# Kernel optimization log

Hardware: AMD Instinct MI355X
Metric: run time of the kernel (lower is better)

## Reference

```python
import jax, jax.numpy as jnp
import numpy as np

NUM_HEADS = 8
EPS = 1e-12  # torch F.normalize default eps


def _l2norm(t):
    # t / max(||t||_2, eps) along last axis (matches F.normalize)
    n = jnp.sqrt(jnp.sum(t * t, axis=-1, keepdims=True))
    return t / jnp.maximum(n, EPS)


def setup_inputs() -> dict:
    key = jax.random.key(0)
    k1, k2, k3 = jax.random.split(key, 3)
    B, N, C = 8, 1024, 768
    x = jax.random.normal(k1, (B, N, C), dtype=jnp.float32)
    w_qkv = jax.random.normal(k2, (C, 3 * C), dtype=jnp.float32) * 0.02
    temperature = jnp.ones((NUM_HEADS, 1, 1), dtype=jnp.float32)
    w_proj = jax.random.normal(k3, (C, C), dtype=jnp.float32) * 0.02
    b_proj = jnp.zeros((C,), dtype=jnp.float32)
    return {"x": x, "w_qkv": w_qkv, "temperature": temperature,
            "w_proj": w_proj, "b_proj": b_proj}


def reference(x, w_qkv, temperature, w_proj, b_proj):
    B, N, C = x.shape
    H = NUM_HEADS
    hd = C // H
    # qkv projection (no bias), split into q,k,v of shape [B,H,N,hd]
    qkv = (x @ w_qkv).reshape(B, N, 3, H, hd)
    qkv = jnp.transpose(qkv, (2, 0, 3, 1, 4))  # [3,B,H,N,hd]
    q, k, v = qkv[0], qkv[1], qkv[2]
    q = _l2norm(q)
    k = _l2norm(k)
    # NOTE: code (unlike canonical XCA) does NOT transpose q/k, so attn is [B,H,N,N]
    attn = jnp.einsum('bhnd,bhmd->bhnm', q, k) * temperature  # temp broadcasts over B
    attn = jax.nn.softmax(attn, axis=-1)
    out = jnp.einsum('bhnm,bhmd->bhnd', attn, v)  # [B,H,N,hd]
    out = jnp.transpose(out, (0, 2, 1, 3)).reshape(B, N, C)
    return out @ w_proj + b_proj
```

## Files before the change

kernel.cpp:

```cpp
#include <hip/hip_runtime.h>
#include <math.h>

typedef __attribute__((ext_vector_type(8))) short bf16x8;
typedef __attribute__((ext_vector_type(4))) float f32x4;
typedef unsigned short u16;
typedef unsigned int u32;


__device__ __forceinline__ u16 f2b(float f) {
  u32 u = __float_as_uint(f);
  return (u16)((u + 0x7fffu + ((u >> 16) & 1u)) >> 16);
}
__device__ __forceinline__ float b2f(u16 h) {
  return __uint_as_float(((u32)h) << 16);
}
__device__ __forceinline__ int swz(int m) { return (m ^ (m >> 2)) & 3; }

__device__ __forceinline__ void async16(const void* g, void* l) {
  __builtin_amdgcn_global_load_lds((const __attribute__((address_space(1))) u32*)g,
                                   (__attribute__((address_space(3))) u32*)l, 16, 0, 0);
}

__global__ __launch_bounds__(256) void prep_kernel(const float* __restrict__ x,
                                                   const float* __restrict__ w_qkv,
                                                   const float* __restrict__ w_proj,
                                                   u16* __restrict__ xb,
                                                   u16* __restrict__ wqkvT,
                                                   u16* __restrict__ wprojT) {
  __shared__ float t[32][33];
  const int blk = blockIdx.x;
  if (blk < 6144) {
    const int idx = blk * 256 + threadIdx.x;
    const float4 v = ((const float4*)x)[idx];
    uint2 o;
    o.x = (u32)f2b(v.x) | ((u32)f2b(v.y) << 16);
    o.y = (u32)f2b(v.z) | ((u32)f2b(v.w) << 16);
    ((uint2*)xb)[idx] = o;
    return;
  }
  const float* in; u16* out; int R, C, bx, by;
  if (blk < 6144 + 1728) {
    const int rem = blk - 6144;
    in = w_qkv; out = wqkvT; R = 768; C = 2304; bx = rem % 72; by = rem / 72;
  } else {
    const int rem = blk - 6144 - 1728;
    in = w_proj; out = wprojT; R = 768; C = 768; bx = rem % 24; by = rem / 24;
  }
  const int c0 = bx * 32, r0 = by * 32;
  const int tc = threadIdx.x & 31, tr = threadIdx.x >> 5;
#pragma unroll
  for (int j = 0; j < 4; ++j)
    t[tr + j * 8][tc] = in[(size_t)(r0 + tr + j * 8) * C + c0 + tc];
  __syncthreads();
#pragma unroll
  for (int j = 0; j < 4; ++j)
    out[(size_t)(c0 + tr + j * 8) * R + r0 + tc] = f2b(t[tc][tr + j * 8]);
}

template<int NT>
__device__ __forceinline__ void gemm_core(const u16* __restrict__ A,
                                          const u16* __restrict__ Bt,
                                          int m0, int n0, f32x4 acc[4][NT / 32]) {
  constexpr int JT = NT / 32;
  constexpr int NINST = (512 + NT * 4) / 256;
  __shared__ u16 Sm[(512 + NT * 4) * 8];
  const int tid = threadIdx.x;
  const int w = tid >> 6, lane = tid & 63;
  const int i15 = lane & 15, quad = lane >> 4;
  const int wm = (w >> 1) * 64, wn = (w & 1) * (NT / 2);
  const int sw = quad ^ swz(i15);

#pragma unroll
  for (int i = 0; i < 4; ++i)
#pragma unroll
    for (int j = 0; j < JT; ++j) acc[i][j] = (f32x4){0.f, 0.f, 0.f, 0.f};

  for (int k0 = 0; k0 < 768; k0 += 32) {
    __syncthreads();
#pragma unroll
    for (int inst = 0; inst < NINST; ++inst) {
      const int s = inst * 256 + tid;
      const u16* src;
      if (inst < 2) {
        const int m = s >> 2, e = s & 3;
        src = A + ((size_t)(m0 + m) * 768 + k0 + (e ^ swz(m)) * 8);
      } else {
        const int s2 = s - 512;
        const int n = s2 >> 2, e = s2 & 3;
        src = Bt + ((size_t)(n0 + n) * 768 + k0 + (e ^ swz(n)) * 8);
      }
      async16(src, (void*)(Sm + (size_t)(inst * 256 + w * 64) * 8));
    }
    __syncthreads();
    bf16x8 af[4], bf[JT];
#pragma unroll
    for (int i = 0; i < 4; ++i)
      af[i] = *(const bf16x8*)(Sm + ((size_t)(wm + i * 16 + i15) * 4 + sw) * 8);
#pragma unroll
    for (int j = 0; j < JT; ++j)
      bf[j] = *(const bf16x8*)(Sm + ((size_t)512 + (wn + j * 16 + i15) * 4 + sw) * 8);
#pragma unroll
    for (int i = 0; i < 4; ++i)
#pragma unroll
      for (int j = 0; j < JT; ++j)
        acc[i][j] = __builtin_amdgcn_mfma_f32_16x16x32_bf16(af[i], bf[j], acc[i][j], 0, 0, 0);
  }
}

__global__ __launch_bounds__(256, 3) void qkv_gemm_kernel(
    const u16* __restrict__ xb, const u16* __restrict__ wT,
    const float* __restrict__ temp,
    u16* __restrict__ q, u16* __restrict__ k, u16* __restrict__ vT) {
  f32x4 acc[4][6];
  const int bid = blockIdx.x;
  const int xcd = bid & 7, slot = bid >> 3;
  const int mb = xcd * 8 + slot / 12, nb = slot % 12;
  const int m0 = mb * 128, n0 = nb * 192;
  gemm_core<192>(xb, wT, m0, n0, acc);

  const int tid = threadIdx.x, w = tid >> 6, lane = tid & 63;
  const int i15 = lane & 15, quad = lane >> 4;
  const int wm = (w >> 1) * 64;
  const int three = nb >> 2;
  const int h = ((nb & 3) << 1) + (w & 1);

  if (three < 2) {
    u16* dst = three ? k : q;
    const float sc_extra = three ? 1.f : temp[h];
#pragma unroll
    for (int it = 0; it < 4; ++it) {
#pragma unroll
      for (int r = 0; r < 4; ++r) {
        float s = 0.f;
#pragma unroll
        for (int jt = 0; jt < 6; ++jt) s += acc[it][jt][r] * acc[it][jt][r];
        s += __shfl_xor(s, 1); s += __shfl_xor(s, 2);
        s += __shfl_xor(s, 4); s += __shfl_xor(s, 8);
        const float scale = sc_extra / fmaxf(sqrtf(s), 1e-12f);
        const int m = m0 + wm + it * 16 + quad * 4 + r;
        const int b = m >> 10, n = m & 1023;
        u16* rowp = dst + ((size_t)(b * 8 + h) * 1024 + n) * 96;
#pragma unroll
        for (int jt = 0; jt < 6; ++jt)
          rowp[jt * 16 + i15] = f2b(acc[it][jt][r] * scale);
      }
    }
  } else {
#pragma unroll
    for (int it = 0; it < 4; ++it) {
      const int mb4 = m0 + wm + it * 16 + quad * 4;
      const int b = mb4 >> 10, nbase = mb4 & 1023;
#pragma unroll
      for (int jt = 0; jt < 6; ++jt) {
        const int d = jt * 16 + i15;
        uint2 pk;
        pk.x = (u32)f2b(acc[it][jt][0]) | ((u32)f2b(acc[it][jt][1]) << 16);
        pk.y = (u32)f2b(acc[it][jt][2]) | ((u32)f2b(acc[it][jt][3]) << 16);
        *(uint2*)(vT + ((size_t)(b * 8 + h) * 96 + d) * 1024 + nbase) = pk;
      }
    }
  }
}

__global__ __launch_bounds__(256, 2) void attn_kernel(
    const u16* __restrict__ q, const u16* __restrict__ kk,
    const u16* __restrict__ vT, u16* __restrict__ ctx) {
  __shared__ u16 smem[20480];
  u16* KVs = smem;
  const int tid = threadIdx.x, w = tid >> 6, lane = tid & 63;
  const int i15 = lane & 15, quad = lane >> 4;
  const int xs = swz(i15);
  const int bh = blockIdx.x & 63, qbase = (blockIdx.x >> 6) * 128;
  const int b = bh >> 3, h = bh & 7;
  u16* Pw = smem + 12288 + w * 2048;

  bf16x8 qf[2][3];
#pragma unroll
  for (int rt = 0; rt < 2; ++rt) {
    const int qrow = qbase + w * 32 + rt * 16 + i15;
    const u16* qp = q + ((size_t)bh * 1024 + qrow) * 96 + quad * 8;
#pragma unroll
    for (int c = 0; c < 3; ++c) qf[rt][c] = *(const bf16x8*)(qp + c * 32);
  }

  f32x4 o[2][6];
#pragma unroll
  for (int rt = 0; rt < 2; ++rt)
#pragma unroll
    for (int dt = 0; dt < 6; ++dt) o[rt][dt] = (f32x4){0.f, 0.f, 0.f, 0.f};
  float l[2] = {0.f, 0.f};

  const int key_s = tid >> 2, qs = tid & 3;
  const int kgq = qs ^ swz(key_s);
  int vd[3], vc2[3], vgq[3];
  vd[0] = tid >> 2;                      vc2[0] = 0;
  vd[1] = (tid < 128) ? (tid >> 2) + 64 : (tid >> 2) - 32;  vc2[1] = (tid >= 128);
  vd[2] = (tid >> 2) + 32;               vc2[2] = 1;
#pragma unroll
  for (int j = 0; j < 3; ++j) vgq[j] = qs ^ swz(vd[j]);

  uint4 kreg[3], vreg[3];
#pragma unroll
  for (int j = 0; j < 3; ++j) {
    kreg[j] = *(const uint4*)(kk + ((size_t)bh * 1024 + key_s) * 96 + (j * 4 + kgq) * 8);
    vreg[j] = *(const uint4*)(vT + ((size_t)bh * 96 + vd[j]) * 1024 + vc2[j] * 32 + vgq[j] * 8);
  }

  for (int t = 0; t < 16; ++t) {
    __syncthreads();
#pragma unroll
    for (int j = 0; j < 3; ++j) {
      *(uint4*)(KVs + (size_t)(j * 256 + tid) * 8) = kreg[j];
      *(uint4*)(KVs + (size_t)(768 + j * 256 + tid) * 8) = vreg[j];
    }
    __syncthreads();
    if (t < 15) {
      const int kt0 = (t + 1) * 64;
#pragma unroll
      for (int j = 0; j < 3; ++j) {
        kreg[j] = *(const uint4*)(kk + ((size_t)bh * 1024 + kt0 + key_s) * 96 + (j * 4 + kgq) * 8);
        vreg[j] = *(const uint4*)(vT + ((size_t)bh * 96 + vd[j]) * 1024 + kt0 + vc2[j] * 32 + vgq[j] * 8);
      }
    }
#pragma unroll
    for (int kt = 0; kt < 4; ++kt) {
      bf16x8 af[3];
#pragma unroll
      for (int c = 0; c < 3; ++c)
        af[c] = *(const bf16x8*)(KVs + ((size_t)((c * 64 + kt * 16 + i15) * 4) + (quad ^ xs)) * 8);
#pragma unroll
      for (int rt = 0; rt < 2; ++rt) {
        f32x4 s = (f32x4){0.f, 0.f, 0.f, 0.f};
#pragma unroll
        for (int c = 0; c < 3; ++c)
          s = __builtin_amdgcn_mfma_f32_16x16x32_bf16(af[c], qf[rt][c], s, 0, 0, 0);
        const float e0 = __expf(s[0]), e1 = __expf(s[1]);
        const float e2 = __expf(s[2]), e3 = __expf(s[3]);
        l[rt] += (e0 + e1) + (e2 + e3);
        uint2 pk;
        pk.x = (u32)f2b(e0) | ((u32)f2b(e1) << 16);
        pk.y = (u32)f2b(e2) | ((u32)f2b(e3) << 16);
        const int pg = (kt & 1) * 2 + (quad >> 1);
        *(uint2*)(Pw + (size_t)(((kt >> 1) * 32 + rt * 16 + i15) * 4 + (pg ^ xs)) * 8
                      + (quad & 1) * 4) = pk;
      }
    }
#pragma unroll
    for (int c2 = 0; c2 < 2; ++c2) {
      bf16x8 pa[2];
#pragma unroll
      for (int rt = 0; rt < 2; ++rt)
        pa[rt] = *(const bf16x8*)(Pw + (size_t)((c2 * 32 + rt * 16 + i15) * 4 + (quad ^ xs)) * 8);
#pragma unroll
      for (int dt = 0; dt < 6; ++dt) {
        const bf16x8 vb = *(const bf16x8*)(KVs +
            ((size_t)(768 + (c2 * 96 + dt * 16 + i15) * 4) + (quad ^ xs)) * 8);
#pragma unroll
        for (int rt = 0; rt < 2; ++rt)
          o[rt][dt] = __builtin_amdgcn_mfma_f32_16x16x32_bf16(pa[rt], vb, o[rt][dt], 0, 0, 0);
      }
    }
  }

  l[0] += __shfl_xor(l[0], 16); l[0] += __shfl_xor(l[0], 32);
  l[1] += __shfl_xor(l[1], 16); l[1] += __shfl_xor(l[1], 32);
  __syncthreads();
  u16* scr = smem + w * 5120;
#pragma unroll
  for (int rt = 0; rt < 2; ++rt) {
#pragma unroll
    for (int r = 0; r < 4; ++r) {
      const float linv = 1.f / __shfl(l[rt], quad * 4 + r);
      const int row32 = rt * 16 + quad * 4 + r;
#pragma unroll
      for (int dt = 0; dt < 6; ++dt)
        scr[row32 * 104 + dt * 16 + i15] = f2b(o[rt][dt][r] * linv);
    }
  }
#pragma unroll
  for (int jj = 0; jj < 6; ++jj) {
    const int id = jj * 64 + lane;
    const int row32 = id / 12, g = id - row32 * 12;
    const int grow = b * 1024 + qbase + w * 32 + row32;
    *(uint4*)(ctx + (size_t)grow * 768 + h * 96 + g * 8) =
        *(const uint4*)(scr + row32 * 104 + g * 8);
  }
}

__global__ __launch_bounds__(256, 4) void proj_gemm_kernel(
    const u16* __restrict__ ctx, const u16* __restrict__ wT,
    const float* __restrict__ bias, float* __restrict__ out) {
  f32x4 acc[4][2];
  const int bid = blockIdx.x;
  const int xcd = bid & 7, slot = bid >> 3;
  const int mb = xcd * 8 + slot / 12, nb = slot % 12;
  const int m0 = mb * 128, n0 = nb * 64;
  gemm_core<64>(ctx, wT, m0, n0, acc);

  const int tid = threadIdx.x, w = tid >> 6, lane = tid & 63;
  const int i15 = lane & 15, quad = lane >> 4;
  const int wm = (w >> 1) * 64, wn = (w & 1) * 32;
#pragma unroll
  for (int jt = 0; jt < 2; ++jt) {
    const int c = n0 + wn + jt * 16 + i15;
    const float bb = bias[c];
#pragma unroll
    for (int it = 0; it < 4; ++it) {
#pragma unroll
      for (int r = 0; r < 4; ++r) {
        const int m = m0 + wm + it * 16 + quad * 4 + r;
        out[(size_t)m * 768 + c] = acc[it][jt][r] + bb;
      }
    }
  }
}

extern "C" void kernel_launch(void* const* d_in, const int* in_sizes, int n_in,
                              void* d_out, int out_size, void* d_ws, size_t ws_size,
                              hipStream_t stream) {
  const float* x      = (const float*)d_in[0];
  const float* w_qkv  = (const float*)d_in[1];
  const float* temp   = (const float*)d_in[2];
  const float* w_proj = (const float*)d_in[3];
  const float* b_proj = (const float*)d_in[4];

  u16* ws      = (u16*)d_ws;
  u16* xb      = ws;
  u16* wqkvT   = xb + 6291456;
  u16* qb      = wqkvT + 1769472;
  u16* kb      = qb + 6291456;
  u16* vTb     = kb + 6291456;
  u16* ctxb    = vTb + 6291456;
  u16* wprojT  = ctxb + 6291456;

  prep_kernel<<<8448, 256, 0, stream>>>(x, w_qkv, w_proj, xb, wqkvT, wprojT);
  qkv_gemm_kernel<<<768, 256, 0, stream>>>(xb, wqkvT, temp, qb, kb, vTb);
  attn_kernel<<<512, 256, 0, stream>>>(qb, kb, vTb, ctxb);
  proj_gemm_kernel<<<768, 256, 0, stream>>>(ctxb, wprojT, b_proj, (float*)d_out);
}
```

Measured before the change: 209.3 us.

## Halve attention query tile to 64 rows per block and raise occupancy

```diff
diff --git a/kernel.cpp b/kernel.cpp
--- a/kernel.cpp
+++ b/kernel.cpp
@@ -162,33 +162,30 @@
   }
 }
 
-__global__ __launch_bounds__(256, 2) void attn_kernel(
+__global__ __launch_bounds__(256, 4) void attn_kernel(
     const u16* __restrict__ q, const u16* __restrict__ kk,
     const u16* __restrict__ vT, u16* __restrict__ ctx) {
-  __shared__ u16 smem[20480];
+  __shared__ u16 smem[16384];
   u16* KVs = smem;
   const int tid = threadIdx.x, w = tid >> 6, lane = tid & 63;
   const int i15 = lane & 15, quad = lane >> 4;
   const int xs = swz(i15);
-  const int bh = blockIdx.x & 63, qbase = (blockIdx.x >> 6) * 128;
+  const int bh = blockIdx.x & 63, qbase = (blockIdx.x >> 6) * 64;
   const int b = bh >> 3, h = bh & 7;
-  u16* Pw = smem + 12288 + w * 2048;
-
-  bf16x8 qf[2][3];
-#pragma unroll
-  for (int rt = 0; rt < 2; ++rt) {
-    const int qrow = qbase + w * 32 + rt * 16 + i15;
+  u16* Pw = smem + 12288 + w * 1024;
+
+  bf16x8 qf[3];
+  {
+    const int qrow = qbase + w * 16 + i15;
     const u16* qp = q + ((size_t)bh * 1024 + qrow) * 96 + quad * 8;
 #pragma unroll
-    for (int c = 0; c < 3; ++c) qf[rt][c] = *(const bf16x8*)(qp + c * 32);
-  }
-
-  f32x4 o[2][6];
-#pragma unroll
-  for (int rt = 0; rt < 2; ++rt)
-#pragma unroll
-    for (int dt = 0; dt < 6; ++dt) o[rt][dt] = (f32x4){0.f, 0.f, 0.f, 0.f};
-  float l[2] = {0.f, 0.f};
+    for (int c = 0; c < 3; ++c) qf[c] = *(const bf16x8*)(qp + c * 32);
+  }
+
+  f32x4 o[6];
+#pragma unroll
+  for (int dt = 0; dt < 6; ++dt) o[dt] = (f32x4){0.f, 0.f, 0.f, 0.f};
+  float l = 0.f;
 
   const int key_s = tid >> 2, qs = tid & 3;
   const int kgq = qs ^ swz(key_s);
@@ -228,62 +225,54 @@
 #pragma unroll
       for (int c = 0; c < 3; ++c)
         af[c] = *(const bf16x8*)(KVs + ((size_t)((c * 64 + kt * 16 + i15) * 4) + (quad ^ xs)) * 8);
-#pragma unroll
-      for (int rt = 0; rt < 2; ++rt) {
-        f32x4 s = (f32x4){0.f, 0.f, 0.f, 0.f};
-#pragma unroll
-        for (int c = 0; c < 3; ++c)
-          s = __builtin_amdgcn_mfma_f32_16x16x32_bf16(af[c], qf[rt][c], s, 0, 0, 0);
-        const float e0 = __expf(s[0]), e1 = __expf(s[1]);
-        const float e2 = __expf(s[2]), e3 = __expf(s[3]);
-        l[rt] += (e0 + e1) + (e2 + e3);
-        uint2 pk;
-        pk.x = (u32)f2b(e0) | ((u32)f2b(e1) << 16);
-        pk.y = (u32)f2b(e2) | ((u32)f2b(e3) << 16);
-        const int pg = (kt & 1) * 2 + (quad >> 1);
-        *(uint2*)(Pw + (size_t)(((kt >> 1) * 32 + rt * 16 + i15) * 4 + (pg ^ xs)) * 8
-                      + (quad & 1) * 4) = pk;
-      }
+      f32x4 s = (f32x4){0.f, 0.f, 0.f, 0.f};
+      __builtin_amdgcn_s_setprio(1);
+#pragma unroll
+      for (int c = 0; c < 3; ++c)
+        s = __builtin_amdgcn_mfma_f32_16x16x32_bf16(af[c], qf[c], s, 0, 0, 0);
+      __builtin_amdgcn_s_setprio(0);
+      const float e0 = __expf(s[0]), e1 = __expf(s[1]);
+      const float e2 = __expf(s[2]), e3 = __expf(s[3]);
+      l += (e0 + e1) + (e2 + e3);
+      uint2 pk;
+      pk.x = (u32)f2b(e0) | ((u32)f2b(e1) << 16);
+      pk.y = (u32)f2b(e2) | ((u32)f2b(e3) << 16);
+      const int pg = (kt & 1) * 2 + (quad >> 1);
+      *(uint2*)(Pw + (size_t)(((kt >> 1) * 16 + i15) * 4 + (pg ^ xs)) * 8
+                    + (quad & 1) * 4) = pk;
     }
 #pragma unroll
     for (int c2 = 0; c2 < 2; ++c2) {
-      bf16x8 pa[2];
-#pragma unroll
-      for (int rt = 0; rt < 2; ++rt)
-        pa[rt] = *(const bf16x8*)(Pw + (size_t)((c2 * 32 + rt * 16 + i15) * 4 + (quad ^ xs)) * 8);
+      const bf16x8 pa = *(const bf16x8*)(Pw + (size_t)((c2 * 16 + i15) * 4 + (quad ^ xs)) * 8);
+      __builtin_amdgcn_s_setprio(1);
 #pragma unroll
       for (int dt = 0; dt < 6; ++dt) {
         const bf16x8 vb = *(const bf16x8*)(KVs +
             ((size_t)(768 + (c2 * 96 + dt * 16 + i15) * 4) + (quad ^ xs)) * 8);
-#pragma unroll
-        for (int rt = 0; rt < 2; ++rt)
-          o[rt][dt] = __builtin_amdgcn_mfma_f32_16x16x32_bf16(pa[rt], vb, o[rt][dt], 0, 0, 0);
-      }
-    }
-  }
-
-  l[0] += __shfl_xor(l[0], 16); l[0] += __shfl_xor(l[0], 32);
-  l[1] += __shfl_xor(l[1], 16); l[1] += __shfl_xor(l[1], 32);
+        o[dt] = __builtin_amdgcn_mfma_f32_16x16x32_bf16(pa, vb, o[dt], 0, 0, 0);
+      }
+      __builtin_amdgcn_s_setprio(0);
+    }
+  }
+
+  l += __shfl_xor(l, 16); l += __shfl_xor(l, 32);
   __syncthreads();
-  u16* scr = smem + w * 5120;
-#pragma unroll
-  for (int rt = 0; rt < 2; ++rt) {
-#pragma unroll
-    for (int r = 0; r < 4; ++r) {
-      const float linv = 1.f / __shfl(l[rt], quad * 4 + r);
-      const int row32 = rt * 16 + quad * 4 + r;
-#pragma unroll
-      for (int dt = 0; dt < 6; ++dt)
-        scr[row32 * 104 + dt * 16 + i15] = f2b(o[rt][dt][r] * linv);
-    }
-  }
-#pragma unroll
-  for (int jj = 0; jj < 6; ++jj) {
+  u16* scr = smem + w * 1664;
+#pragma unroll
+  for (int r = 0; r < 4; ++r) {
+    const float linv = 1.f / __shfl(l, quad * 4 + r);
+    const int row16 = quad * 4 + r;
+#pragma unroll
+    for (int dt = 0; dt < 6; ++dt)
+      scr[row16 * 104 + dt * 16 + i15] = f2b(o[dt][r] * linv);
+  }
+#pragma unroll
+  for (int jj = 0; jj < 3; ++jj) {
     const int id = jj * 64 + lane;
-    const int row32 = id / 12, g = id - row32 * 12;
-    const int grow = b * 1024 + qbase + w * 32 + row32;
+    const int row16 = id / 12, g = id - row16 * 12;
+    const int grow = b * 1024 + qbase + w * 16 + row16;
     *(uint4*)(ctx + (size_t)grow * 768 + h * 96 + g * 8) =
-        *(const uint4*)(scr + row32 * 104 + g * 8);
+        *(const uint4*)(scr + row16 * 104 + g * 8);
   }
 }
 
@@ -335,6 +324,6 @@
 
   prep_kernel<<<8448, 256, 0, stream>>>(x, w_qkv, w_proj, xb, wqkvT, wprojT);
   qkv_gemm_kernel<<<768, 256, 0, stream>>>(xb, wqkvT, temp, qb, kb, vTb);
-  attn_kernel<<<512, 256, 0, stream>>>(qb, kb, vTb, ctxb);
+  attn_kernel<<<1024, 256, 0, stream>>>(qb, kb, vTb, ctxb);
   proj_gemm_kernel<<<768, 256, 0, stream>>>(ctxb, wprojT, b_proj, (float*)d_out);
 }
```

Result: slower. 261.0 us (+24.7%).
